# Performance work log

Measured on AMD Instinct MI355X. Metric: run time of the kernel, lower is better.

## Reference

```python
import jax, jax.numpy as jnp
import numpy as np

N, D, B, C, T, TOD = 8192, 32, 2, 8, 12, 288
PARAM_SCALE = 0.3  # keep relu+softmax logits well-conditioned (original uses plain randn init)


def setup_inputs() -> dict:
    key = jax.random.key(0)
    k0, k1, k2, k3, k4 = jax.random.split(key, 5)
    return {
        "x": jax.random.normal(k0, (B, C, N, T), dtype=jnp.float32),
        "nodevec1": PARAM_SCALE * jax.random.normal(k1, (N, D), dtype=jnp.float32),
        "nodevec2": PARAM_SCALE * jax.random.normal(k2, (N, D), dtype=jnp.float32),
        "timevec": PARAM_SCALE * jax.random.normal(k3, (TOD, D), dtype=jnp.float32),
        "k": PARAM_SCALE * jax.random.normal(k4, (D, D, D), dtype=jnp.float32),
        "time_ind": 100,
    }


def reference(x, nodevec1, nodevec2, timevec, k, time_ind):
    # Dynamic Tucker-decomposition adjacency (SpatialGraphConv.forward, eval mode -> dropout is identity)
    tv = timevec[time_ind]                             # [D]   time_vec
    core = jnp.einsum('d,def->ef', tv, k)              # [D,D] adp1 (squeezed)
    # adp2/adp3 chain: (nodevec1 @ core) @ nodevec2.T  -> [N,N]
    adp = jnp.einsum('ne,ef->nf', nodevec1, core)      # [N,D]
    adp = jnp.einsum('nf,mf->nm', adp, nodevec2)       # [N,N]
    adp = jax.nn.softmax(jax.nn.relu(adp), axis=-1)    # row-softmax over neighbors
    # NConv: neighbor aggregation  'bcnt,nm->bcmt'
    return jnp.einsum('bcnt,nm->bcmt', x, adp)
```

## Files before the change

kernel.cpp:

```cpp
#include <hip/hip_runtime.h>
#include <hip/hip_bf16.h>


#define NN 8192
#define DD 32
#define TT 12
#define NSPLIT 8
#define CHUNK 1024
#define ESTR 72

typedef __attribute__((ext_vector_type(8))) short bf16x8;
typedef __attribute__((ext_vector_type(4))) short bf16x4;
typedef __attribute__((ext_vector_type(4))) float f32x4;

static __device__ __forceinline__ unsigned short f2bf(float f) {
  unsigned int u = __float_as_uint(f);
  u = (u + 0x7FFFu + ((u >> 16) & 1u)) >> 16;
  return (unsigned short)u;
}

static __device__ __forceinline__ float fexp2(float x) {
#if __has_builtin(__builtin_amdgcn_exp2f)
  return __builtin_amdgcn_exp2f(x);
#else
  return __builtin_exp2f(x);
#endif
}

__global__ __launch_bounds__(256) void k_prep(const float* __restrict__ nv1,
                                              const float* __restrict__ nv2,
                                              const float* __restrict__ timevec,
                                              const float* __restrict__ kk,
                                              const int* __restrict__ tind,
                                              unsigned short* __restrict__ t1b,
                                              unsigned short* __restrict__ nv2b) {
  __shared__ float cs[1024];
  const int tid = threadIdx.x;
  const float* tv = timevec + (size_t)tind[0] * DD;
  for (int idx = tid; idx < 1024; idx += 256) {
    float acc = 0.f;
#pragma unroll
    for (int d = 0; d < DD; ++d) acc += tv[d] * kk[d * 1024 + idx];
    cs[idx] = acc;
  }
  __syncthreads();
  const int nbase = blockIdx.x * 128;
  const int f = tid & 31, sub = tid >> 5;
#pragma unroll 4
  for (int it = 0; it < 16; ++it) {
    const int n = nbase + it * 8 + sub;
    const float* nr = nv1 + (size_t)n * DD;
    float acc = 0.f;
#pragma unroll
    for (int e = 0; e < DD; ++e) acc += nr[e] * cs[e * DD + f];
    t1b[(size_t)n * DD + f] = f2bf(acc * 1.4426950408889634f);
  }
#pragma unroll 4
  for (int it = 0; it < 16; ++it) {
    const int idx = nbase * DD + it * 256 + tid;
    nv2b[idx] = f2bf(nv2[idx]);
  }
}

__global__ __launch_bounds__(256) void k_stats(const unsigned short* __restrict__ t1b,
                                               const unsigned short* __restrict__ nv2b,
                                               float* __restrict__ sums) {
  const int tid = threadIdx.x;
  const int w = tid >> 6, lane = tid & 63, q = lane >> 4, i16 = lane & 15;
  const int nbase = blockIdx.x * 64 + w * 16;
  bf16x8 a = *(const bf16x8*)(t1b + (size_t)(nbase + i16) * DD + q * 8);
  const f32x4 z4 = {0.f, 0.f, 0.f, 0.f};
  float s[4] = {0.f, 0.f, 0.f, 0.f};
  const int m0 = blockIdx.y * 1024;
  for (int mt = m0; mt < m0 + 1024; mt += 64) {
#pragma unroll
    for (int u = 0; u < 4; ++u) {
      bf16x8 b = *(const bf16x8*)(nv2b + (size_t)(mt + u * 16 + i16) * DD + q * 8);
      f32x4 d = __builtin_amdgcn_mfma_f32_16x16x32_bf16(a, b, z4, 0, 0, 0);
#pragma unroll
      for (int r = 0; r < 4; ++r) s[r] += fexp2(fmaxf(d[r], 0.f));
    }
  }
#pragma unroll
  for (int r = 0; r < 4; ++r)
    for (int off = 1; off < 16; off <<= 1) s[r] += __shfl_xor(s[r], off, 64);
  if (i16 == 0) {
#pragma unroll
    for (int r = 0; r < 4; ++r) atomicAdd(&sums[nbase + q * 4 + r], s[r]);
  }
}

__global__ __launch_bounds__(256) void k_y(const float* __restrict__ x,
                                           const float* __restrict__ sums,
                                           unsigned short* __restrict__ yT) {
  __shared__ float xs[3072];
  const int tid = threadIdx.x;
  const int n0 = blockIdx.x * 256;
  const int bc = blockIdx.y;
  const float* xp = x + (size_t)bc * NN * TT + (size_t)n0 * TT;
#pragma unroll
  for (int j = 0; j < 12; ++j) xs[j * 256 + tid] = xp[j * 256 + tid];
  __syncthreads();
  const float rinv = 1.0f / sums[n0 + tid];
#pragma unroll
  for (int t = 0; t < 12; ++t)
    yT[(size_t)(bc * TT + t) * NN + n0 + tid] = f2bf(xs[tid * 12 + t] * rinv);
}

__global__ __launch_bounds__(512, 4) void k_mega(const unsigned short* __restrict__ t1b,
                                                 const unsigned short* __restrict__ nv2b,
                                                 const unsigned short* __restrict__ yT,
                                                 float* __restrict__ part) {
  const int tid = threadIdx.x;
  const int w = tid >> 6, lane = tid & 63, q = lane >> 4, i16 = lane & 15;
  const int wc = w >> 1, wm = w & 1;
  const int mb = blockIdx.x * 128;
  const int nt0 = blockIdx.y * CHUNK;

  __shared__ unsigned short Ew[2][128][ESTR];

  const bf16x8 bg = *(const bf16x8*)(nv2b + (size_t)(mb + w * 16 + i16) * DD + q * 8);

  const f32x4 z4 = {0.f, 0.f, 0.f, 0.f};
  f32x4 acc[3][4];
#pragma unroll
  for (int c = 0; c < 3; ++c)
#pragma unroll
    for (int ms = 0; ms < 4; ++ms) acc[c][ms] = (f32x4){0.f, 0.f, 0.f, 0.f};

#pragma unroll
  for (int s = 0; s < 4; ++s) {
    bf16x8 at = *(const bf16x8*)(t1b + (size_t)(nt0 + s * 16 + i16) * DD + q * 8);
    f32x4 d = __builtin_amdgcn_mfma_f32_16x16x32_bf16(at, bg, z4, 0, 0, 0);
    bf16x4 e;
#pragma unroll
    for (int r = 0; r < 4; ++r) e[r] = (short)f2bf(fexp2(fmaxf(d[r], 0.f)));
    *(bf16x4*)&Ew[0][w * 16 + i16][s * 16 + q * 4] = e;
  }
  __syncthreads();

  int p = 0;
  for (int st = 0; st < 16; ++st, p ^= 1) {
    const int nt = nt0 + st * 64;
    const bool more = (st < 15);

    bf16x8 atn[4];
    if (more) {
#pragma unroll
      for (int s = 0; s < 4; ++s)
        atn[s] = *(const bf16x8*)(t1b + (size_t)(nt + 64 + s * 16 + i16) * DD + q * 8);
    }

    bf16x8 yfr[3], efr[4];
#pragma unroll
    for (int c = 0; c < 3; ++c)
      yfr[c] = *(const bf16x8*)(yT + (size_t)((wc * 3 + c) * 16 + i16) * NN + nt + q * 8);
#pragma unroll
    for (int ms = 0; ms < 4; ++ms)
      efr[ms] = *(const bf16x8*)&Ew[p][wm * 64 + ms * 16 + i16][q * 8];

    f32x4 d0, d1;
    if (more) {
      d0 = __builtin_amdgcn_mfma_f32_16x16x32_bf16(atn[0], bg, z4, 0, 0, 0);
      d1 = __builtin_amdgcn_mfma_f32_16x16x32_bf16(atn[1], bg, z4, 0, 0, 0);
    }

#pragma unroll
    for (int c = 0; c < 3; ++c)
#pragma unroll
      for (int ms = 0; ms < 4; ++ms)
        acc[c][ms] = __builtin_amdgcn_mfma_f32_16x16x32_bf16(yfr[c], efr[ms], acc[c][ms], 0, 0, 0);

    if (more) {
      bf16x4 e0, e1;
#pragma unroll
      for (int r = 0; r < 4; ++r) {
        e0[r] = (short)f2bf(fexp2(fmaxf(d0[r], 0.f)));
        e1[r] = (short)f2bf(fexp2(fmaxf(d1[r], 0.f)));
      }
      *(bf16x4*)&Ew[p ^ 1][w * 16 + i16][q * 4] = e0;
      *(bf16x4*)&Ew[p ^ 1][w * 16 + i16][16 + q * 4] = e1;
      f32x4 d2 = __builtin_amdgcn_mfma_f32_16x16x32_bf16(atn[2], bg, z4, 0, 0, 0);
      f32x4 d3 = __builtin_amdgcn_mfma_f32_16x16x32_bf16(atn[3], bg, z4, 0, 0, 0);
      bf16x4 e2, e3;
#pragma unroll
      for (int r = 0; r < 4; ++r) {
        e2[r] = (short)f2bf(fexp2(fmaxf(d2[r], 0.f)));
        e3[r] = (short)f2bf(fexp2(fmaxf(d3[r], 0.f)));
      }
      *(bf16x4*)&Ew[p ^ 1][w * 16 + i16][32 + q * 4] = e2;
      *(bf16x4*)&Ew[p ^ 1][w * 16 + i16][48 + q * 4] = e3;
    }

#pragma unroll
    for (int c = 0; c < 3; ++c)
      yfr[c] = *(const bf16x8*)(yT + (size_t)((wc * 3 + c) * 16 + i16) * NN + nt + 32 + q * 8);
#pragma unroll
    for (int ms = 0; ms < 4; ++ms)
      efr[ms] = *(const bf16x8*)&Ew[p][wm * 64 + ms * 16 + i16][32 + q * 8];
#pragma unroll
    for (int c = 0; c < 3; ++c)
#pragma unroll
      for (int ms = 0; ms < 4; ++ms)
        acc[c][ms] = __builtin_amdgcn_mfma_f32_16x16x32_bf16(yfr[c], efr[ms], acc[c][ms], 0, 0, 0);

    __syncthreads();
  }

  float* pp = part + (size_t)blockIdx.y * 192 * NN;
#pragma unroll
  for (int c = 0; c < 3; ++c)
#pragma unroll
    for (int ms = 0; ms < 4; ++ms) {
      const int colbase = (wc * 3 + c) * 16 + q * 4;
      const int m = mb + wm * 64 + ms * 16 + i16;
#pragma unroll
      for (int r = 0; r < 4; ++r)
        pp[(size_t)(colbase + r) * NN + m] = acc[c][ms][r];
    }
}

__global__ __launch_bounds__(256) void k_reduce(const float* __restrict__ part,
                                                float* __restrict__ out) {
  __shared__ float os[3072];
  const int tid = threadIdx.x;
  const int m0 = blockIdx.x * 256;
  const int bc = blockIdx.y;
#pragma unroll
  for (int t = 0; t < 12; ++t) {
    const int col = bc * TT + t;
    float s = 0.f;
#pragma unroll
    for (int nc = 0; nc < NSPLIT; ++nc)
      s += part[((size_t)nc * 192 + col) * NN + m0 + tid];
    os[tid * 12 + t] = s;
  }
  __syncthreads();
  float* op = out + (size_t)bc * NN * TT + (size_t)m0 * TT;
#pragma unroll
  for (int j = 0; j < 12; ++j) op[j * 256 + tid] = os[j * 256 + tid];
}

extern "C" void kernel_launch(void* const* d_in, const int* in_sizes, int n_in,
                              void* d_out, int out_size, void* d_ws, size_t ws_size,
                              hipStream_t stream) {
  const float* x = (const float*)d_in[0];
  const float* nv1 = (const float*)d_in[1];
  const float* nv2 = (const float*)d_in[2];
  const float* tv = (const float*)d_in[3];
  const float* kk = (const float*)d_in[4];
  const int* tind = (const int*)d_in[5];
  float* out = (float*)d_out;

  char* ws = (char*)d_ws;
  unsigned short* t1b  = (unsigned short*)(ws);
  unsigned short* nv2b = (unsigned short*)(ws + 524288);
  float* sums          = (float*)(ws + 1048576);
  unsigned short* yT   = (unsigned short*)(ws + 1081344);
  float* part          = (float*)(ws + 4227072);

  hipMemsetAsync(sums, 0, NN * sizeof(float), stream);
  k_prep<<<64, 256, 0, stream>>>(nv1, nv2, tv, kk, tind, t1b, nv2b);
  k_stats<<<dim3(128, 8), 256, 0, stream>>>(t1b, nv2b, sums);
  k_y<<<dim3(32, 16), 256, 0, stream>>>(x, sums, yT);
  k_mega<<<dim3(64, NSPLIT), 512, 0, stream>>>(t1b, nv2b, yT, part);
  k_reduce<<<dim3(32, 16), 256, 0, stream>>>(part, out);
}
```

Measured before the change: 180.8 us.

## Fuse all stages into one cooperative persistent kernel with grid barriers

Merges the prep, stats, y-scaling, main GEMM and reduce kernels into a single cooperative kernel of 512 blocks, separated by a software grid barrier built on atomics. The aim is to remove the launch gaps and tail drain between the five kernels and the separate memset. The trade-offs are grid-wide barrier cost, uneven per-phase work across blocks, and a fixed block mapping. If cooperative launch fails, it falls back to the original multi-kernel path.

Measured after the change: 613.9 us. 3.4x slower.

```diff
diff --git a/kernel.cpp b/kernel.cpp
--- a/kernel.cpp
+++ b/kernel.cpp
@@ -8,6 +8,7 @@
 #define NSPLIT 8
 #define CHUNK 1024
 #define ESTR 72
+#define NBLK 512
 
 typedef __attribute__((ext_vector_type(8))) short bf16x8;
 typedef __attribute__((ext_vector_type(4))) short bf16x4;
@@ -25,6 +26,241 @@
 #else
   return __builtin_exp2f(x);
 #endif
+}
+
+static __device__ __forceinline__ void gridsync(int* bar) {
+  __syncthreads();
+  if (threadIdx.x == 0) {
+    __threadfence();
+    int gen = __hip_atomic_load(&bar[1], __ATOMIC_RELAXED, __HIP_MEMORY_SCOPE_AGENT);
+    int arr = __hip_atomic_fetch_add(&bar[0], 1, __ATOMIC_ACQ_REL, __HIP_MEMORY_SCOPE_AGENT);
+    if (arr == NBLK - 1) {
+      __hip_atomic_store(&bar[0], 0, __ATOMIC_RELAXED, __HIP_MEMORY_SCOPE_AGENT);
+      __hip_atomic_fetch_add(&bar[1], 1, __ATOMIC_RELEASE, __HIP_MEMORY_SCOPE_AGENT);
+    } else {
+      while (__hip_atomic_load(&bar[1], __ATOMIC_ACQUIRE, __HIP_MEMORY_SCOPE_AGENT) == gen)
+        __builtin_amdgcn_s_sleep(1);
+    }
+    __threadfence();
+  }
+  __syncthreads();
+}
+
+__global__ __launch_bounds__(512, 4) void k_all(
+    const float* __restrict__ x, const float* __restrict__ nv1,
+    const float* __restrict__ nv2, const float* __restrict__ timevec,
+    const float* __restrict__ kk, const int* __restrict__ tind,
+    unsigned short* __restrict__ t1b, unsigned short* __restrict__ nv2b,
+    float* __restrict__ sums, unsigned short* __restrict__ yT,
+    float* __restrict__ part, float* __restrict__ out, int* __restrict__ bar) {
+  __shared__ __align__(16) unsigned char smem[2 * 128 * ESTR * 2];
+  const int tid = threadIdx.x;
+  const int b = blockIdx.x;
+  const int w = tid >> 6, lane = tid & 63, q = lane >> 4, i16 = lane & 15;
+  const f32x4 z4 = {0.f, 0.f, 0.f, 0.f};
+
+  if (tid < 16) sums[b * 16 + tid] = 0.f;
+  if (b < 64) {
+    float* cs = (float*)smem;
+    const float* tv = timevec + (size_t)tind[0] * DD;
+    for (int idx = tid; idx < 1024; idx += 512) {
+      float acc = 0.f;
+#pragma unroll
+      for (int d = 0; d < DD; ++d) acc += tv[d] * kk[d * 1024 + idx];
+      cs[idx] = acc;
+    }
+    __syncthreads();
+    const int nbase = b * 128;
+    const int f = tid & 31, sub = tid >> 5;
+#pragma unroll 4
+    for (int it = 0; it < 8; ++it) {
+      const int n = nbase + it * 16 + sub;
+      const float* nr = nv1 + (size_t)n * DD;
+      float acc = 0.f;
+#pragma unroll
+      for (int e = 0; e < DD; ++e) acc += nr[e] * cs[e * DD + f];
+      t1b[(size_t)n * DD + f] = f2bf(acc * 1.4426950408889634f);
+    }
+#pragma unroll 4
+    for (int it = 0; it < 8; ++it) {
+      const int idx = nbase * DD + it * 512 + tid;
+      nv2b[idx] = f2bf(nv2[idx]);
+    }
+  }
+  gridsync(bar);
+
+  {
+    const int nbase = (b & 127) * 64 + (w & 3) * 16;
+    const int m0 = (b >> 7) * 2048 + (w >> 2) * 1024;
+    bf16x8 a = *(const bf16x8*)(t1b + (size_t)(nbase + i16) * DD + q * 8);
+    float s[4] = {0.f, 0.f, 0.f, 0.f};
+    for (int mt = m0; mt < m0 + 1024; mt += 64) {
+#pragma unroll
+      for (int u = 0; u < 4; ++u) {
+        bf16x8 bb = *(const bf16x8*)(nv2b + (size_t)(mt + u * 16 + i16) * DD + q * 8);
+        f32x4 d = __builtin_amdgcn_mfma_f32_16x16x32_bf16(a, bb, z4, 0, 0, 0);
+#pragma unroll
+        for (int r = 0; r < 4; ++r) s[r] += fexp2(fmaxf(d[r], 0.f));
+      }
+    }
+#pragma unroll
+    for (int r = 0; r < 4; ++r)
+      for (int off = 1; off < 16; off <<= 1) s[r] += __shfl_xor(s[r], off, 64);
+    if (i16 == 0) {
+#pragma unroll
+      for (int r = 0; r < 4; ++r) atomicAdd(&sums[nbase + q * 4 + r], s[r]);
+    }
+  }
+  gridsync(bar);
+
+  {
+    float* xs = (float*)smem;
+    float* rs = (float*)smem + 3072;
+    const int n0 = (b & 31) * 256;
+    const int bc = b >> 5;
+    const float* xp = x + (size_t)bc * NN * TT + (size_t)n0 * TT;
+#pragma unroll
+    for (int j = 0; j < 6; ++j) xs[j * 512 + tid] = xp[j * 512 + tid];
+    if (tid < 256) rs[tid] = 1.0f / sums[n0 + tid];
+    __syncthreads();
+#pragma unroll
+    for (int j = 0; j < 6; ++j) {
+      const int idx = j * 512 + tid;
+      const int t = idx >> 8, i = idx & 255;
+      yT[(size_t)(bc * TT + t) * NN + n0 + i] = f2bf(xs[i * TT + t] * rs[i]);
+    }
+  }
+  gridsync(bar);
+
+  {
+    typedef unsigned short EwRow[ESTR];
+    EwRow* Ew0 = (EwRow*)smem;
+    EwRow* Ew1 = (EwRow*)smem + 128;
+    const int wc = w >> 1, wm = w & 1;
+    const int mb = (b >> 3) * 128;
+    const int nt0 = (b & 7) * CHUNK;
+
+    const bf16x8 bg = *(const bf16x8*)(nv2b + (size_t)(mb + w * 16 + i16) * DD + q * 8);
+
+    f32x4 acc[3][4];
+#pragma unroll
+    for (int c = 0; c < 3; ++c)
+#pragma unroll
+      for (int ms = 0; ms < 4; ++ms) acc[c][ms] = (f32x4){0.f, 0.f, 0.f, 0.f};
+
+#pragma unroll
+    for (int s = 0; s < 4; ++s) {
+      bf16x8 at = *(const bf16x8*)(t1b + (size_t)(nt0 + s * 16 + i16) * DD + q * 8);
+      f32x4 d = __builtin_amdgcn_mfma_f32_16x16x32_bf16(at, bg, z4, 0, 0, 0);
+      bf16x4 e;
+#pragma unroll
+      for (int r = 0; r < 4; ++r) e[r] = (short)f2bf(fexp2(fmaxf(d[r], 0.f)));
+      *(bf16x4*)&Ew0[w * 16 + i16][s * 16 + q * 4] = e;
+    }
+    __syncthreads();
+
+    for (int st = 0; st < 16; ++st) {
+      EwRow* Ecur = (st & 1) ? Ew1 : Ew0;
+      EwRow* Enxt = (st & 1) ? Ew0 : Ew1;
+      const int nt = nt0 + st * 64;
+      const bool more = (st < 15);
+
+      bf16x8 atn[4];
+      if (more) {
+#pragma unroll
+        for (int s = 0; s < 4; ++s)
+          atn[s] = *(const bf16x8*)(t1b + (size_t)(nt + 64 + s * 16 + i16) * DD + q * 8);
+      }
+
+      bf16x8 yfr[3], efr[4];
+#pragma unroll
+      for (int c = 0; c < 3; ++c)
+        yfr[c] = *(const bf16x8*)(yT + (size_t)((wc * 3 + c) * 16 + i16) * NN + nt + q * 8);
+#pragma unroll
+      for (int ms = 0; ms < 4; ++ms)
+        efr[ms] = *(const bf16x8*)&Ecur[wm * 64 + ms * 16 + i16][q * 8];
+
+      f32x4 d0, d1;
+      if (more) {
+        d0 = __builtin_amdgcn_mfma_f32_16x16x32_bf16(atn[0], bg, z4, 0, 0, 0);
+        d1 = __builtin_amdgcn_mfma_f32_16x16x32_bf16(atn[1], bg, z4, 0, 0, 0);
+      }
+
+#pragma unroll
+      for (int c = 0; c < 3; ++c)
+#pragma unroll
+        for (int ms = 0; ms < 4; ++ms)
+          acc[c][ms] = __builtin_amdgcn_mfma_f32_16x16x32_bf16(yfr[c], efr[ms], acc[c][ms], 0, 0, 0);
+
+      if (more) {
+        bf16x4 e0, e1;
+#pragma unroll
+        for (int r = 0; r < 4; ++r) {
+          e0[r] = (short)f2bf(fexp2(fmaxf(d0[r], 0.f)));
+          e1[r] = (short)f2bf(fexp2(fmaxf(d1[r], 0.f)));
+        }
+        *(bf16x4*)&Enxt[w * 16 + i16][q * 4] = e0;
+        *(bf16x4*)&Enxt[w * 16 + i16][16 + q * 4] = e1;
+        f32x4 d2 = __builtin_amdgcn_mfma_f32_16x16x32_bf16(atn[2], bg, z4, 0, 0, 0);
+        f32x4 d3 = __builtin_amdgcn_mfma_f32_16x16x32_bf16(atn[3], bg, z4, 0, 0, 0);
+        bf16x4 e2, e3;
+#pragma unroll
+        for (int r = 0; r < 4; ++r) {
+          e2[r] = (short)f2bf(fexp2(fmaxf(d2[r], 0.f)));
+          e3[r] = (short)f2bf(fexp2(fmaxf(d3[r], 0.f)));
+        }
+        *(bf16x4*)&Enxt[w * 16 + i16][32 + q * 4] = e2;
+        *(bf16x4*)&Enxt[w * 16 + i16][48 + q * 4] = e3;
+      }
+
+#pragma unroll
+      for (int c = 0; c < 3; ++c)
+        yfr[c] = *(const bf16x8*)(yT + (size_t)((wc * 3 + c) * 16 + i16) * NN + nt + 32 + q * 8);
+#pragma unroll
+      for (int ms = 0; ms < 4; ++ms)
+        efr[ms] = *(const bf16x8*)&Ecur[wm * 64 + ms * 16 + i16][32 + q * 8];
+#pragma unroll
+      for (int c = 0; c < 3; ++c)
+#pragma unroll
+        for (int ms = 0; ms < 4; ++ms)
+          acc[c][ms] = __builtin_amdgcn_mfma_f32_16x16x32_bf16(yfr[c], efr[ms], acc[c][ms], 0, 0, 0);
+
+      __syncthreads();
+    }
+
+    float* pp = part + (size_t)(b & 7) * 192 * NN;
+#pragma unroll
+    for (int c = 0; c < 3; ++c)
+#pragma unroll
+      for (int ms = 0; ms < 4; ++ms) {
+        const int colbase = (wc * 3 + c) * 16 + q * 4;
+        const int m = mb + wm * 64 + ms * 16 + i16;
+#pragma unroll
+        for (int r = 0; r < 4; ++r)
+          pp[(size_t)(colbase + r) * NN + m] = acc[c][ms][r];
+      }
+  }
+  gridsync(bar);
+
+  {
+    float* os = (float*)smem;
+    const int m0 = (b & 31) * 256;
+    const int bc = b >> 5;
+    const int ml = tid & 255, th = tid >> 8;
+#pragma unroll
+    for (int t = th * 6; t < th * 6 + 6; ++t) {
+      const int col = bc * TT + t;
+      float s = 0.f;
+#pragma unroll
+      for (int nc = 0; nc < NSPLIT; ++nc)
+        s += part[((size_t)nc * 192 + col) * NN + m0 + ml];
+      os[ml * TT + t] = s;
+    }
+    __syncthreads();
+    float* op = out + (size_t)bc * NN * TT + (size_t)m0 * TT;
+#pragma unroll
+    for (int j = 0; j < 6; ++j) op[j * 512 + tid] = os[j * 512 + tid];
+  }
 }
 
 __global__ __launch_bounds__(256) void k_prep(const float* __restrict__ nv1,
@@ -116,18 +352,14 @@
   const int wc = w >> 1, wm = w & 1;
   const int mb = blockIdx.x * 128;
   const int nt0 = blockIdx.y * CHUNK;
-
   __shared__ unsigned short Ew[2][128][ESTR];
-
   const bf16x8 bg = *(const bf16x8*)(nv2b + (size_t)(mb + w * 16 + i16) * DD + q * 8);
-
   const f32x4 z4 = {0.f, 0.f, 0.f, 0.f};
   f32x4 acc[3][4];
 #pragma unroll
   for (int c = 0; c < 3; ++c)
 #pragma unroll
     for (int ms = 0; ms < 4; ++ms) acc[c][ms] = (f32x4){0.f, 0.f, 0.f, 0.f};
-
 #pragma unroll
   for (int s = 0; s < 4; ++s) {
     bf16x8 at = *(const bf16x8*)(t1b + (size_t)(nt0 + s * 16 + i16) * DD + q * 8);
@@ -138,19 +370,16 @@
     *(bf16x4*)&Ew[0][w * 16 + i16][s * 16 + q * 4] = e;
   }
   __syncthreads();
-
   int p = 0;
   for (int st = 0; st < 16; ++st, p ^= 1) {
     const int nt = nt0 + st * 64;
     const bool more = (st < 15);
-
     bf16x8 atn[4];
     if (more) {
 #pragma unroll
       for (int s = 0; s < 4; ++s)
         atn[s] = *(const bf16x8*)(t1b + (size_t)(nt + 64 + s * 16 + i16) * DD + q * 8);
     }
-
     bf16x8 yfr[3], efr[4];
 #pragma unroll
     for (int c = 0; c < 3; ++c)
@@ -158,19 +387,16 @@
 #pragma unroll
     for (int ms = 0; ms < 4; ++ms)
       efr[ms] = *(const bf16x8*)&Ew[p][wm * 64 + ms * 16 + i16][q * 8];
-
     f32x4 d0, d1;
     if (more) {
       d0 = __builtin_amdgcn_mfma_f32_16x16x32_bf16(atn[0], bg, z4, 0, 0, 0);
       d1 = __builtin_amdgcn_mfma_f32_16x16x32_bf16(atn[1], bg, z4, 0, 0, 0);
     }
-
 #pragma unroll
     for (int c = 0; c < 3; ++c)
 #pragma unroll
       for (int ms = 0; ms < 4; ++ms)
         acc[c][ms] = __builtin_amdgcn_mfma_f32_16x16x32_bf16(yfr[c], efr[ms], acc[c][ms], 0, 0, 0);
-
     if (more) {
       bf16x4 e0, e1;
 #pragma unroll
@@ -191,7 +417,6 @@
       *(bf16x4*)&Ew[p ^ 1][w * 16 + i16][32 + q * 4] = e2;
       *(bf16x4*)&Ew[p ^ 1][w * 16 + i16][48 + q * 4] = e3;
     }
-
 #pragma unroll
     for (int c = 0; c < 3; ++c)
       yfr[c] = *(const bf16x8*)(yT + (size_t)((wc * 3 + c) * 16 + i16) * NN + nt + 32 + q * 8);
@@ -203,10 +428,8 @@
 #pragma unroll
       for (int ms = 0; ms < 4; ++ms)
         acc[c][ms] = __builtin_amdgcn_mfma_f32_16x16x32_bf16(yfr[c], efr[ms], acc[c][ms], 0, 0, 0);
-
     __syncthreads();
   }
-
   float* pp = part + (size_t)blockIdx.y * 192 * NN;
 #pragma unroll
   for (int c = 0; c < 3; ++c)
@@ -258,11 +481,23 @@
   float* sums          = (float*)(ws + 1048576);
   unsigned short* yT   = (unsigned short*)(ws + 1081344);
   float* part          = (float*)(ws + 4227072);
-
-  hipMemsetAsync(sums, 0, NN * sizeof(float), stream);
-  k_prep<<<64, 256, 0, stream>>>(nv1, nv2, tv, kk, tind, t1b, nv2b);
-  k_stats<<<dim3(128, 8), 256, 0, stream>>>(t1b, nv2b, sums);
-  k_y<<<dim3(32, 16), 256, 0, stream>>>(x, sums, yT);
-  k_mega<<<dim3(64, NSPLIT), 512, 0, stream>>>(t1b, nv2b, yT, part);
-  k_reduce<<<dim3(32, 16), 256, 0, stream>>>(part, out);
-}
+  int* bar             = (int*)(ws + 54558720);
+
+  hipMemsetAsync(bar, 0, 64, stream);
+
+  void* args[] = {(void*)&x,    (void*)&nv1, (void*)&nv2,  (void*)&tv,
+                  (void*)&kk,   (void*)&tind, (void*)&t1b, (void*)&nv2b,
+                  (void*)&sums, (void*)&yT,   (void*)&part, (void*)&out,
+                  (void*)&bar};
+  hipError_t e = hipLaunchCooperativeKernel((const void*)k_all, dim3(NBLK),
+                                            dim3(512), args, 0, stream);
+  if (e != hipSuccess) {
+    (void)hipGetLastError();
+    hipMemsetAsync(sums, 0, NN * sizeof(float), stream);
+    k_prep<<<64, 256, 0, stream>>>(nv1, nv2, tv, kk, tind, t1b, nv2b);
+    k_stats<<<dim3(128, 8), 256, 0, stream>>>(t1b, nv2b, sums);
+    k_y<<<dim3(32, 16), 256, 0, stream>>>(x, sums, yT);
+    k_mega<<<dim3(64, NSPLIT), 512, 0, stream>>>(t1b, nv2b, yT, part);
+    k_reduce<<<dim3(32, 16), 256, 0, stream>>>(part, out);
+  }
+}
```

## Deepen k_mega pipeline to 128-wide stages with XOR-swizzled LDS and fold memset

Applied to the files above, without the earlier changes.

The main kernel now handles 128 neighbour columns per stage instead of 64, which halves the number of barriers. It also software-pipelines the yT global loads so that each 32-column slice is fetched one step ahead of its MFMA use, and interleaves the next stage's exp computation between the accumulation MFMAs. The padded LDS row stride is replaced by an XOR swizzle on a 128-wide tile to avoid bank conflicts. The separate memset of sums is folded into k_prep, which saves one launch. In exchange, LDS use per block and register pressure both rise, which may cut occupancy at the current launch bounds.

Measured after the change: 180.8 us. Within noise of the previous version (+0.0%).

```diff
diff --git a/kernel.cpp b/kernel.cpp
--- a/kernel.cpp
+++ b/kernel.cpp
@@ -7,7 +7,6 @@
 #define TT 12
 #define NSPLIT 8
 #define CHUNK 1024
-#define ESTR 72
 
 typedef __attribute__((ext_vector_type(8))) short bf16x8;
 typedef __attribute__((ext_vector_type(4))) short bf16x4;
@@ -33,9 +32,11 @@
                                               const float* __restrict__ kk,
                                               const int* __restrict__ tind,
                                               unsigned short* __restrict__ t1b,
-                                              unsigned short* __restrict__ nv2b) {
+                                              unsigned short* __restrict__ nv2b,
+                                              float* __restrict__ sums) {
   __shared__ float cs[1024];
   const int tid = threadIdx.x;
+  if (tid < 128) sums[blockIdx.x * 128 + tid] = 0.f;
   const float* tv = timevec + (size_t)tind[0] * DD;
   for (int idx = tid; idx < 1024; idx += 256) {
     float acc = 0.f;
@@ -107,6 +108,7 @@
     yT[(size_t)(bc * TT + t) * NN + n0 + tid] = f2bf(xs[tid * 12 + t] * rinv);
 }
 
+#define SWC(c) ((c) ^ swz)
 __global__ __launch_bounds__(512, 4) void k_mega(const unsigned short* __restrict__ t1b,
                                                  const unsigned short* __restrict__ nv2b,
                                                  const unsigned short* __restrict__ yT,
@@ -116,10 +118,12 @@
   const int wc = w >> 1, wm = w & 1;
   const int mb = blockIdx.x * 128;
   const int nt0 = blockIdx.y * CHUNK;
-
-  __shared__ unsigned short Ew[2][128][ESTR];
+  const int swz = (i16 & 7) << 3;
+
+  __shared__ unsigned short Ew[2][128][128];
 
   const bf16x8 bg = *(const bf16x8*)(nv2b + (size_t)(mb + w * 16 + i16) * DD + q * 8);
+  const int rowm = w * 16 + i16;
 
   const f32x4 z4 = {0.f, 0.f, 0.f, 0.f};
   f32x4 acc[3][4];
@@ -128,82 +132,136 @@
 #pragma unroll
     for (int ms = 0; ms < 4; ++ms) acc[c][ms] = (f32x4){0.f, 0.f, 0.f, 0.f};
 
-#pragma unroll
-  for (int s = 0; s < 4; ++s) {
-    bf16x8 at = *(const bf16x8*)(t1b + (size_t)(nt0 + s * 16 + i16) * DD + q * 8);
-    f32x4 d = __builtin_amdgcn_mfma_f32_16x16x32_bf16(at, bg, z4, 0, 0, 0);
-    bf16x4 e;
-#pragma unroll
-    for (int r = 0; r < 4; ++r) e[r] = (short)f2bf(fexp2(fmaxf(d[r], 0.f)));
-    *(bf16x4*)&Ew[0][w * 16 + i16][s * 16 + q * 4] = e;
-  }
+  const unsigned short* yp[3];
+#pragma unroll
+  for (int c = 0; c < 3; ++c)
+    yp[c] = yT + (size_t)((wc * 3 + c) * 16 + i16) * NN + q * 8;
+
+#pragma unroll
+  for (int g = 0; g < 4; ++g) {
+    bf16x8 a0 = *(const bf16x8*)(t1b + (size_t)(nt0 + g * 32 + i16) * DD + q * 8);
+    bf16x8 a1 = *(const bf16x8*)(t1b + (size_t)(nt0 + g * 32 + 16 + i16) * DD + q * 8);
+    f32x4 d0 = __builtin_amdgcn_mfma_f32_16x16x32_bf16(a0, bg, z4, 0, 0, 0);
+    f32x4 d1 = __builtin_amdgcn_mfma_f32_16x16x32_bf16(a1, bg, z4, 0, 0, 0);
+    bf16x4 e0, e1;
+#pragma unroll
+    for (int r = 0; r < 4; ++r) {
+      e0[r] = (short)f2bf(fexp2(fmaxf(d0[r], 0.f)));
+      e1[r] = (short)f2bf(fexp2(fmaxf(d1[r], 0.f)));
+    }
+    *(bf16x4*)&Ew[0][rowm][SWC(g * 32 + q * 4)] = e0;
+    *(bf16x4*)&Ew[0][rowm][SWC(g * 32 + 16 + q * 4)] = e1;
+  }
+  bf16x8 y0[3];
+#pragma unroll
+  for (int c = 0; c < 3; ++c) y0[c] = *(const bf16x8*)(yp[c] + nt0);
   __syncthreads();
 
-  int p = 0;
-  for (int st = 0; st < 16; ++st, p ^= 1) {
-    const int nt = nt0 + st * 64;
-    const bool more = (st < 15);
-
-    bf16x8 atn[4];
-    if (more) {
-#pragma unroll
-      for (int s = 0; s < 4; ++s)
-        atn[s] = *(const bf16x8*)(t1b + (size_t)(nt + 64 + s * 16 + i16) * DD + q * 8);
-    }
-
-    bf16x8 yfr[3], efr[4];
+  for (int st = 0; st < 8; ++st) {
+    const int p = st & 1;
+    const int nt = nt0 + st * 128;
+    const bool more = (st < 7);
+    const unsigned short(*Ec)[128] = Ew[p];
+    unsigned short(*En)[128] = Ew[p ^ 1];
+
+    bf16x8 at[8];
+    if (more) {
+#pragma unroll
+      for (int s = 0; s < 8; ++s)
+        at[s] = *(const bf16x8*)(t1b + (size_t)(nt + 128 + s * 16 + i16) * DD + q * 8);
+    }
+
+    bf16x8 efr[4], y1[3], y2[3], y3[3];
+#pragma unroll
+    for (int ms = 0; ms < 4; ++ms)
+      efr[ms] = *(const bf16x8*)&Ec[wm * 64 + ms * 16 + i16][SWC(q * 8)];
+#pragma unroll
+    for (int c = 0; c < 3; ++c) y1[c] = *(const bf16x8*)(yp[c] + nt + 32);
 #pragma unroll
     for (int c = 0; c < 3; ++c)
-      yfr[c] = *(const bf16x8*)(yT + (size_t)((wc * 3 + c) * 16 + i16) * NN + nt + q * 8);
-#pragma unroll
-    for (int ms = 0; ms < 4; ++ms)
-      efr[ms] = *(const bf16x8*)&Ew[p][wm * 64 + ms * 16 + i16][q * 8];
-
-    f32x4 d0, d1;
-    if (more) {
-      d0 = __builtin_amdgcn_mfma_f32_16x16x32_bf16(atn[0], bg, z4, 0, 0, 0);
-      d1 = __builtin_amdgcn_mfma_f32_16x16x32_bf16(atn[1], bg, z4, 0, 0, 0);
-    }
-
-#pragma unroll
-    for (int c = 0; c < 3; ++c)
 #pragma unroll
       for (int ms = 0; ms < 4; ++ms)
-        acc[c][ms] = __builtin_amdgcn_mfma_f32_16x16x32_bf16(yfr[c], efr[ms], acc[c][ms], 0, 0, 0);
-
-    if (more) {
+        acc[c][ms] = __builtin_amdgcn_mfma_f32_16x16x32_bf16(y0[c], efr[ms], acc[c][ms], 0, 0, 0);
+    if (more) {
+      f32x4 d0 = __builtin_amdgcn_mfma_f32_16x16x32_bf16(at[0], bg, z4, 0, 0, 0);
+      f32x4 d1 = __builtin_amdgcn_mfma_f32_16x16x32_bf16(at[1], bg, z4, 0, 0, 0);
       bf16x4 e0, e1;
 #pragma unroll
       for (int r = 0; r < 4; ++r) {
         e0[r] = (short)f2bf(fexp2(fmaxf(d0[r], 0.f)));
         e1[r] = (short)f2bf(fexp2(fmaxf(d1[r], 0.f)));
       }
-      *(bf16x4*)&Ew[p ^ 1][w * 16 + i16][q * 4] = e0;
-      *(bf16x4*)&Ew[p ^ 1][w * 16 + i16][16 + q * 4] = e1;
-      f32x4 d2 = __builtin_amdgcn_mfma_f32_16x16x32_bf16(atn[2], bg, z4, 0, 0, 0);
-      f32x4 d3 = __builtin_amdgcn_mfma_f32_16x16x32_bf16(atn[3], bg, z4, 0, 0, 0);
-      bf16x4 e2, e3;
+      *(bf16x4*)&En[rowm][SWC(q * 4)] = e0;
+      *(bf16x4*)&En[rowm][SWC(16 + q * 4)] = e1;
+    }
+#pragma unroll
+    for (int ms = 0; ms < 4; ++ms)
+      efr[ms] = *(const bf16x8*)&Ec[wm * 64 + ms * 16 + i16][SWC(32 + q * 8)];
+#pragma unroll
+    for (int c = 0; c < 3; ++c) y2[c] = *(const bf16x8*)(yp[c] + nt + 64);
+#pragma unroll
+    for (int c = 0; c < 3; ++c)
+#pragma unroll
+      for (int ms = 0; ms < 4; ++ms)
+        acc[c][ms] = __builtin_amdgcn_mfma_f32_16x16x32_bf16(y1[c], efr[ms], acc[c][ms], 0, 0, 0);
+    if (more) {
+      f32x4 d0 = __builtin_amdgcn_mfma_f32_16x16x32_bf16(at[2], bg, z4, 0, 0, 0);
+      f32x4 d1 = __builtin_amdgcn_mfma_f32_16x16x32_bf16(at[3], bg, z4, 0, 0, 0);
+      bf16x4 e0, e1;
 #pragma unroll
       for (int r = 0; r < 4; ++r) {
-        e2[r] = (short)f2bf(fexp2(fmaxf(d2[r], 0.f)));
-        e3[r] = (short)f2bf(fexp2(fmaxf(d3[r], 0.f)));
+        e0[r] = (short)f2bf(fexp2(fmaxf(d0[r], 0.f)));
+        e1[r] = (short)f2bf(fexp2(fmaxf(d1[r], 0.f)));
       }
-      *(bf16x4*)&Ew[p ^ 1][w * 16 + i16][32 + q * 4] = e2;
-      *(bf16x4*)&Ew[p ^ 1][w * 16 + i16][48 + q * 4] = e3;
-    }
-
+      *(bf16x4*)&En[rowm][SWC(32 + q * 4)] = e0;
+      *(bf16x4*)&En[rowm][SWC(48 + q * 4)] = e1;
+    }
+#pragma unroll
+    for (int ms = 0; ms < 4; ++ms)
+      efr[ms] = *(const bf16x8*)&Ec[wm * 64 + ms * 16 + i16][SWC(64 + q * 8)];
+#pragma unroll
+    for (int c = 0; c < 3; ++c) y3[c] = *(const bf16x8*)(yp[c] + nt + 96);
 #pragma unroll
     for (int c = 0; c < 3; ++c)
-      yfr[c] = *(const bf16x8*)(yT + (size_t)((wc * 3 + c) * 16 + i16) * NN + nt + 32 + q * 8);
+#pragma unroll
+      for (int ms = 0; ms < 4; ++ms)
+        acc[c][ms] = __builtin_amdgcn_mfma_f32_16x16x32_bf16(y2[c], efr[ms], acc[c][ms], 0, 0, 0);
+    if (more) {
+      f32x4 d0 = __builtin_amdgcn_mfma_f32_16x16x32_bf16(at[4], bg, z4, 0, 0, 0);
+      f32x4 d1 = __builtin_amdgcn_mfma_f32_16x16x32_bf16(at[5], bg, z4, 0, 0, 0);
+      bf16x4 e0, e1;
+#pragma unroll
+      for (int r = 0; r < 4; ++r) {
+        e0[r] = (short)f2bf(fexp2(fmaxf(d0[r], 0.f)));
+        e1[r] = (short)f2bf(fexp2(fmaxf(d1[r], 0.f)));
+      }
+      *(bf16x4*)&En[rowm][SWC(64 + q * 4)] = e0;
+      *(bf16x4*)&En[rowm][SWC(80 + q * 4)] = e1;
+    }
 #pragma unroll
     for (int ms = 0; ms < 4; ++ms)
-      efr[ms] = *(const bf16x8*)&Ew[p][wm * 64 + ms * 16 + i16][32 + q * 8];
+      efr[ms] = *(const bf16x8*)&Ec[wm * 64 + ms * 16 + i16][SWC(96 + q * 8)];
+    if (more) {
+#pragma unroll
+      for (int c = 0; c < 3; ++c) y0[c] = *(const bf16x8*)(yp[c] + nt + 128);
+    }
 #pragma unroll
     for (int c = 0; c < 3; ++c)
 #pragma unroll
       for (int ms = 0; ms < 4; ++ms)
-        acc[c][ms] = __builtin_amdgcn_mfma_f32_16x16x32_bf16(yfr[c], efr[ms], acc[c][ms], 0, 0, 0);
-
+        acc[c][ms] = __builtin_amdgcn_mfma_f32_16x16x32_bf16(y3[c], efr[ms], acc[c][ms], 0, 0, 0);
+    if (more) {
+      f32x4 d0 = __builtin_amdgcn_mfma_f32_16x16x32_bf16(at[6], bg, z4, 0, 0, 0);
+      f32x4 d1 = __builtin_amdgcn_mfma_f32_16x16x32_bf16(at[7], bg, z4, 0, 0, 0);
+      bf16x4 e0, e1;
+#pragma unroll
+      for (int r = 0; r < 4; ++r) {
+        e0[r] = (short)f2bf(fexp2(fmaxf(d0[r], 0.f)));
+        e1[r] = (short)f2bf(fexp2(fmaxf(d1[r], 0.f)));
+      }
+      *(bf16x4*)&En[rowm][SWC(96 + q * 4)] = e0;
+      *(bf16x4*)&En[rowm][SWC(112 + q * 4)] = e1;
+    }
     __syncthreads();
   }
 
@@ -259,8 +317,7 @@
   unsigned short* yT   = (unsigned short*)(ws + 1081344);
   float* part          = (float*)(ws + 4227072);
 
-  hipMemsetAsync(sums, 0, NN * sizeof(float), stream);
-  k_prep<<<64, 256, 0, stream>>>(nv1, nv2, tv, kk, tind, t1b, nv2b);
+  k_prep<<<64, 256, 0, stream>>>(nv1, nv2, tv, kk, tind, t1b, nv2b, sums);
   k_stats<<<dim3(128, 8), 256, 0, stream>>>(t1b, nv2b, sums);
   k_y<<<dim3(32, 16), 256, 0, stream>>>(x, sums, yT);
   k_mega<<<dim3(64, NSPLIT), 512, 0, stream>>>(t1b, nv2b, yT, part);
```
